# Optimization experiments

Hardware: AMD Instinct MI355X
Metric: run time of the kernel (lower is better)

## Reference

```python
import jax, jax.numpy as jnp
import numpy as np

HEADS = 16

def setup_inputs() -> dict:
    key = jax.random.key(0)
    ks = jax.random.split(key, 5)
    B, T, D = 2, 2048, 2048
    s = 0.02
    return {
        "x": jax.random.normal(ks[0], (B, T, D), dtype=jnp.float32),
        "Wq": jax.random.normal(ks[1], (D, D), dtype=jnp.float32) * s,
        "Wk": jax.random.normal(ks[2], (D, D), dtype=jnp.float32) * s,
        "Wv": jax.random.normal(ks[3], (D, D), dtype=jnp.float32) * s,
        "Wo": jax.random.normal(ks[4], (D, D), dtype=jnp.float32) * s,
    }

def reference(x, Wq, Wk, Wv, Wo):
    B, T, _ = x.shape
    H = HEADS
    Dh = Wq.shape[1] // H
    # projections: [B,T,H,Dh]
    q = (x @ Wq).reshape(B, T, H, Dh)
    k = (x @ Wk).reshape(B, T, H, Dh)
    v = (x @ Wv).reshape(B, T, H, Dh)
    # raw scores [B,H,T,T]
    scores = jnp.einsum("bthd,bshd->bhts", q, k)
    # NOTE (faithful to source): mask is multiplicative 0/1 tril (the
    # masked_fill(-inf) in the torch code is not in-place and has no effect),
    # and the scale is sqrt(token_len), not sqrt(head_dim).
    mask = jnp.tril(jnp.ones((T, T), dtype=scores.dtype))
    scores = scores * mask
    attn = jax.nn.softmax(scores / (T ** 0.5), axis=-1)
    out = jnp.einsum("bhts,bshd->bthd", attn, v).reshape(B, T, H * Dh)
    return out @ Wo
```

## Files before the change

### kernel.cpp

```cpp
#include <hip/hip_runtime.h>


typedef __attribute__((ext_vector_type(4))) float  f32x4;
typedef __attribute__((ext_vector_type(8))) short  bf16x8;
typedef __attribute__((ext_vector_type(4))) unsigned short u16x4;

#define AS1 __attribute__((address_space(1)))
#define AS3 __attribute__((address_space(3)))

__device__ __forceinline__ void llds16(const void* g, void* l) {
  __builtin_amdgcn_global_load_lds((const AS1 void*)g, (AS3 void*)l, 16, 0, 0);
}

__device__ __forceinline__ unsigned short f2bf(float f) {
  unsigned int u = __builtin_bit_cast(unsigned int, f);
  u += 0x7fffu + ((u >> 16) & 1u);
  return (unsigned short)(u >> 16);
}

__device__ __forceinline__ float bf2f(unsigned short u) {
  return __builtin_bit_cast(float, (unsigned int)u << 16);
}

__global__ __launch_bounds__(256) void cast_x_kernel(const float* __restrict__ in,
                                                     unsigned short* __restrict__ out) {
  int i = blockIdx.x * 256 + threadIdx.x;
  f32x4 v = ((const f32x4*)in)[i];
  u16x4 o;
  o[0] = f2bf(v[0]); o[1] = f2bf(v[1]); o[2] = f2bf(v[2]); o[3] = f2bf(v[3]);
  ((u16x4*)out)[i] = o;
}

__global__ __launch_bounds__(256) void transpose_w_kernel(const float* __restrict__ W,
                                                          unsigned short* __restrict__ Wt) {
  __shared__ float tile[32][33];
  const int bx = blockIdx.x << 5;
  const int by = blockIdx.y << 5;
  const int tx = threadIdx.x;
  const int ty = threadIdx.y;
#pragma unroll
  for (int r = ty; r < 32; r += 8)
    tile[r][tx] = W[(size_t)(bx + r) * 2048 + by + tx];
  __syncthreads();
#pragma unroll
  for (int r = ty; r < 32; r += 8)
    Wt[(size_t)(by + r) * 2048 + bx + tx] = f2bf(tile[tx][r]);
}

template <int OUT>
__global__ __launch_bounds__(512, 2) void gemm_bt(const unsigned short* __restrict__ A,
                                                  const unsigned short* __restrict__ Bt,
                                                  void* __restrict__ Cv) {
  __shared__ __align__(16) char smem[98304];
  const int tid  = threadIdx.x;
  const int lane = tid & 63;
  const int w    = tid >> 6;
  const int f    = blockIdx.x;
  const int xcd  = f & 7;
  const int g    = f >> 3;
  const int bm   = ((xcd >> 1) << 3) + (g & 7);
  const int bn   = ((xcd & 1) << 2) + (g >> 3);
  const int wr = w >> 2, wc = w & 3;
  const int q16 = lane >> 4;
  const int l15 = lane & 15;

  const int aIdx = (w << 6) + lane;
  const int aRow = aIdx >> 2, aCph = aIdx & 3;
  const unsigned short* aSrc = A + (size_t)((bm << 7) + aRow) * 2048
                                 + ((aCph ^ ((aRow >> 1) & 3)) << 3);
  const int bRow0 = aIdx >> 2, bCph0 = aIdx & 3;
  const int bIdx1 = 512 + aIdx;
  const int bRow1 = bIdx1 >> 2, bCph1 = bIdx1 & 3;
  const unsigned short* bSrc0 = Bt + (size_t)((bn << 8) + bRow0) * 2048
                                  + ((bCph0 ^ ((bRow0 >> 1) & 3)) << 3);
  const unsigned short* bSrc1 = Bt + (size_t)((bn << 8) + bRow1) * 2048
                                  + ((bCph1 ^ ((bRow1 >> 1) & 3)) << 3);

  const int swx = ((q16 ^ ((l15 >> 1) & 3)) << 4);
  const int aoff = ((wr << 6) + l15) * 64 + swx;
  const int boff = 8192 + ((wc << 6) + l15) * 64 + swx;

  f32x4 acc[4][4];
#pragma unroll
  for (int i = 0; i < 4; ++i)
#pragma unroll
    for (int j = 0; j < 4; ++j) acc[i][j] = (f32x4){0.f, 0.f, 0.f, 0.f};

  auto stageT = [&](int t, int slot) {
    char* sb = smem + slot * 24576 + (w << 10);
    const size_t ko = (size_t)t << 5;
    llds16(aSrc + ko, sb);
    llds16(bSrc0 + ko, sb + 8192);
    llds16(bSrc1 + ko, sb + 16384);
  };

  auto computeT = [&](int slot) {
    const char* base = smem + slot * 24576;
    bf16x8 af[4], bf[4];
#pragma unroll
    for (int mi = 0; mi < 4; ++mi) af[mi] = *(const bf16x8*)(base + aoff + (mi << 10));
#pragma unroll
    for (int ni = 0; ni < 4; ++ni) bf[ni] = *(const bf16x8*)(base + boff + (ni << 10));
    __builtin_amdgcn_s_setprio(1);
#pragma unroll
    for (int mi = 0; mi < 4; ++mi)
#pragma unroll
      for (int ni = 0; ni < 4; ++ni)
        acc[mi][ni] = __builtin_amdgcn_mfma_f32_16x16x32_bf16(af[mi], bf[ni], acc[mi][ni], 0, 0, 0);
    __builtin_amdgcn_s_setprio(0);
  };

  stageT(0, 0); stageT(1, 1); stageT(2, 2);

#pragma unroll 1
  for (int i = 0; i < 60; i += 4) {
#pragma unroll
    for (int u = 0; u < 4; ++u) {
      stageT(i + u + 3, (u + 3) & 3);
      asm volatile("s_waitcnt vmcnt(9)" ::: "memory");
      __builtin_amdgcn_s_barrier();
      computeT(u);
      __builtin_amdgcn_s_barrier();
    }
  }
  stageT(63, 3);
  asm volatile("s_waitcnt vmcnt(9)" ::: "memory");
  __builtin_amdgcn_s_barrier();
  computeT(0);
  __builtin_amdgcn_s_barrier();
  asm volatile("s_waitcnt vmcnt(6)" ::: "memory");
  __builtin_amdgcn_s_barrier();
  computeT(1);
  __builtin_amdgcn_s_barrier();
  asm volatile("s_waitcnt vmcnt(3)" ::: "memory");
  __builtin_amdgcn_s_barrier();
  computeT(2);
  __builtin_amdgcn_s_barrier();
  asm volatile("s_waitcnt vmcnt(0)" ::: "memory");
  __builtin_amdgcn_s_barrier();
  computeT(3);

  const int rb = q16 << 2;
#pragma unroll
  for (int mi = 0; mi < 4; ++mi) {
    int m0 = (bm << 7) + (wr << 6) + (mi << 4) + rb;
#pragma unroll
    for (int ni = 0; ni < 4; ++ni) {
      int n = (bn << 8) + (wc << 6) + (ni << 4) + l15;
      if constexpr (OUT == 0) {
        unsigned short* C = (unsigned short*)Cv;
#pragma unroll
        for (int j = 0; j < 4; ++j)
          C[(size_t)(m0 + j) * 2048 + n] = f2bf(acc[mi][ni][j]);
      } else if constexpr (OUT == 1) {
        u16x4 pk;
#pragma unroll
        for (int j = 0; j < 4; ++j) pk[j] = f2bf(acc[mi][ni][j]);
        int b = m0 >> 11, t = m0 & 2047;
        unsigned short* C = (unsigned short*)Cv;
        *(u16x4*)(C + ((size_t)((b << 4) + (n >> 7)) * 128 + (n & 127)) * 2048 + t) = pk;
      } else {
        float* C = (float*)Cv;
#pragma unroll
        for (int j = 0; j < 4; ++j)
          C[(size_t)(m0 + j) * 2048 + n] = acc[mi][ni][j];
      }
    }
  }
}

__global__ __launch_bounds__(256) void vsuf_kernel(const unsigned short* __restrict__ Vt,
                                                   float* __restrict__ Suf) {
  const int row  = blockIdx.x * 4 + (threadIdx.x >> 6);
  const int lane = threadIdx.x & 63;
  const unsigned short* vp = Vt + (size_t)row * 2048 + (lane << 5);
  float a = 0.f;
#pragma unroll
  for (int c = 0; c < 4; ++c) {
    bf16x8 v = *(const bf16x8*)(vp + (c << 3));
#pragma unroll
    for (int j = 0; j < 8; ++j) a += bf2f((unsigned short)v[j]);
  }
  float I = a;
#pragma unroll
  for (int off = 1; off < 64; off <<= 1) {
    float t = __shfl_down(I, off, 64);
    I += (lane + off < 64) ? t : 0.f;
  }
  Suf[(size_t)lane * 4096 + row] = I;
  if (lane == 0) Suf[(size_t)64 * 4096 + row] = 0.f;
}

__global__ __launch_bounds__(256) void attn_kernel(const unsigned short* __restrict__ Q,
                                                   const unsigned short* __restrict__ K,
                                                   const unsigned short* __restrict__ V,
                                                   const float* __restrict__ Suf,
                                                   unsigned short* __restrict__ O) {
  __shared__ __align__(16) char smem[36864];
  const int tid  = threadIdx.x;
  const int lane = tid & 63;
  const int w    = tid >> 6;
  const int q16  = lane >> 4;
  const int l15  = lane & 15;
  const int f    = blockIdx.x;
  const int bh    = ((f & 7) << 2) + ((f >> 3) & 3);
  const int strip = 31 - (f >> 5);
  const int b  = bh >> 4;
  const float scale = 0.02209708691207961f;
  const size_t qkbase = ((size_t)(b << 11)) * 2048 + ((size_t)(bh & 15) << 7);
  const size_t vbase  = (size_t)bh << 18;
  const int rb = q16 << 2;
  char* Psm = smem + 32768 + (w << 10);

  const int numIter = 2 * strip + 2;
  const int t0 = (strip << 6) + (w << 4);

  auto stage = [&](int s0, int kb, int vb) {
#pragma unroll
    for (int c = 0; c < 2; ++c) {
      int ch = (w << 1) + c;
      int rowK = (ch << 2) + q16;
      int colbK = (l15 << 4) ^ ((rowK & 7) << 4);
      llds16(K + qkbase + (size_t)(s0 + rowK) * 2048 + (colbK >> 1), smem + kb + (ch << 10));
      int rowV = (ch << 4) + (lane >> 2);
      int colbV = ((lane & 3) << 4) ^ (((rowV >> 2) & 3) << 4);
      llds16(V + vbase + (size_t)rowV * 2048 + s0 + (colbV >> 1), smem + vb + (ch << 10));
    }
  };

  bf16x8 qf[4];
  {
    const unsigned short* qp = Q + qkbase + (size_t)(t0 + l15) * 2048 + (q16 << 3);
#pragma unroll
    for (int kk = 0; kk < 4; ++kk) qf[kk] = *(const bf16x8*)(qp + (kk << 5));
  }

  f32x4 oacc[8];
#pragma unroll
  for (int i = 0; i < 8; ++i) oacc[i] = (f32x4){0.f, 0.f, 0.f, 0.f};
  float ell[4] = {0.f, 0.f, 0.f, 0.f};

  stage(0, 0, 16384);
  asm volatile("s_waitcnt vmcnt(0)" ::: "memory");
  __syncthreads();

  int cur = 0;
  for (int it = 0; it < numIter; ++it) {
    const int s0 = it << 5;
    if (it + 1 < numIter)
      stage(s0 + 32, (cur ^ 1) << 13, 16384 + ((cur ^ 1) << 13));

    if (s0 <= t0) {
      const int kb = cur << 13;
      const int vb = 16384 + (cur << 13);

      f32x4 sA = (f32x4){0.f, 0.f, 0.f, 0.f}, sB = (f32x4){0.f, 0.f, 0.f, 0.f};
#pragma unroll
      for (int kk = 0; kk < 4; ++kk) {
        int r0 = l15;
        bf16x8 k0f = *(const bf16x8*)(smem + kb + (r0 << 8) + (((kk << 6) + (q16 << 4)) ^ ((r0 & 7) << 4)));
        sA = __builtin_amdgcn_mfma_f32_16x16x32_bf16(qf[kk], k0f, sA, 0, 0, 0);
        int r1 = 16 + l15;
        bf16x8 k1f = *(const bf16x8*)(smem + kb + (r1 << 8) + (((kk << 6) + (q16 << 4)) ^ ((r1 & 7) << 4)));
        sB = __builtin_amdgcn_mfma_f32_16x16x32_bf16(qf[kk], k1f, sB, 0, 0, 0);
      }

      float pA[4], pB[4];
#pragma unroll
      for (int j = 0; j < 4; ++j) {
        int t  = t0 + rb + j;
        int sa = s0 + l15;
        float vA = (sa <= t)      ? sA[j] * scale : 0.f;
        float vB = (sa + 16 <= t) ? sB[j] * scale : 0.f;
        pA[j] = __expf(vA);
        pB[j] = __expf(vB);
        ell[j] += pA[j] + pB[j];
      }

#pragma unroll
      for (int j = 0; j < 4; ++j) {
        int r   = rb + j;
        int swz = ((r >> 1) & 3) << 4;
        *(unsigned short*)(Psm + (r << 6) + ((l15 << 1) ^ swz))        = f2bf(pA[j]);
        *(unsigned short*)(Psm + (r << 6) + ((32 + (l15 << 1)) ^ swz)) = f2bf(pB[j]);
      }
      asm volatile("s_waitcnt lgkmcnt(0)" ::: "memory");

      bf16x8 pa;
      {
        int r = l15;
        pa = *(const bf16x8*)(Psm + (r << 6) + ((q16 << 4) ^ (((r >> 1) & 3) << 4)));
      }
#pragma unroll
      for (int ni = 0; ni < 8; ++ni) {
        int dr = (ni << 4) + l15;
        bf16x8 vbf = *(const bf16x8*)(smem + vb + (dr << 6) + ((q16 << 4) ^ (((dr >> 2) & 3) << 4)));
        oacc[ni] = __builtin_amdgcn_mfma_f32_16x16x32_bf16(pa, vbf, oacc[ni], 0, 0, 0);
      }
    }

    asm volatile("s_waitcnt vmcnt(0)" ::: "memory");
    __syncthreads();
    cur ^= 1;
  }

  const int send = (t0 & ~31) + 32;
  const float* sp = Suf + (size_t)(send >> 5) * 4096 + ((size_t)bh << 7);
  const float extra = (float)(2048 - send);
#pragma unroll
  for (int ni = 0; ni < 8; ++ni) {
    float sv = sp[(ni << 4) + l15];
#pragma unroll
    for (int j = 0; j < 4; ++j) oacc[ni][j] += sv;
  }

#pragma unroll
  for (int j = 0; j < 4; ++j) {
    float r = ell[j];
    r += __shfl_xor(r, 1, 64);
    r += __shfl_xor(r, 2, 64);
    r += __shfl_xor(r, 4, 64);
    r += __shfl_xor(r, 8, 64);
    float inv = 1.0f / (r + extra);
    int t = t0 + rb + j;
    unsigned short* op = O + qkbase + (size_t)t * 2048;
#pragma unroll
    for (int ni = 0; ni < 8; ++ni)
      op[(ni << 4) + l15] = f2bf(oacc[ni][j] * inv);
  }
}

extern "C" void kernel_launch(void* const* d_in, const int* in_sizes, int n_in,
                              void* d_out, int out_size, void* d_ws, size_t ws_size,
                              hipStream_t stream) {
  (void)in_sizes; (void)n_in; (void)out_size; (void)ws_size;
  const float* x  = (const float*)d_in[0];
  const float* Wq = (const float*)d_in[1];
  const float* Wk = (const float*)d_in[2];
  const float* Wv = (const float*)d_in[3];
  const float* Wo = (const float*)d_in[4];
  float* out = (float*)d_out;

  char* ws = (char*)d_ws;
  unsigned short* Xb  = (unsigned short*)(ws);
  unsigned short* Wqt = (unsigned short*)(ws + 16777216);
  unsigned short* Wkt = (unsigned short*)(ws + 16777216 + 8388608);
  unsigned short* Wvt = (unsigned short*)(ws + 16777216 + 2 * 8388608);
  unsigned short* Wot = (unsigned short*)(ws + 16777216 + 3 * 8388608);
  unsigned short* Qb  = (unsigned short*)(ws + 50331648);
  unsigned short* Kb  = (unsigned short*)(ws + 67108864);
  unsigned short* Vt  = (unsigned short*)(ws + 83886080);
  unsigned short* Ob  = Xb;
  float*          Suf = (float*)Wqt;

  cast_x_kernel<<<8192, 256, 0, stream>>>(x, Xb);
  {
    dim3 tb(32, 8), tg(64, 64);
    transpose_w_kernel<<<tg, tb, 0, stream>>>(Wq, Wqt);
    transpose_w_kernel<<<tg, tb, 0, stream>>>(Wk, Wkt);
    transpose_w_kernel<<<tg, tb, 0, stream>>>(Wv, Wvt);
    transpose_w_kernel<<<tg, tb, 0, stream>>>(Wo, Wot);
  }
  gemm_bt<0><<<256, 512, 0, stream>>>(Xb, Wqt, (void*)Qb);
  gemm_bt<0><<<256, 512, 0, stream>>>(Xb, Wkt, (void*)Kb);
  gemm_bt<1><<<256, 512, 0, stream>>>(Xb, Wvt, (void*)Vt);

  vsuf_kernel<<<1024, 256, 0, stream>>>(Vt, Suf);

  attn_kernel<<<1024, 256, 0, stream>>>(Qb, Kb, Vt, Suf, Ob);

  gemm_bt<2><<<256, 512, 0, stream>>>(Ob, Wot, (void*)out);
}
```

Baseline: 273.4 us.

## Fuse QKV GEMMs and weight transposes, pipeline GEMM frags, fold scale into Q

Merges the three Q/K/V projection GEMMs into a single 768-block launch. This relies on Wqt/Wkt/Wvt being contiguous so they act as one 6144-row B matrix, with each block routing its epilogue to Q, K or V by region. The four weight transposes become one launch with a z dimension. The GEMM main loop is restructured to use one barrier per step and double-buffered register fragments, so the LDS reads for the next tile overlap the MFMAs of the current one. Attention takes the score scale from Q (pre-scaled in the GEMM epilogue), skips the causal mask on fully unmasked tiles, and uses a cheaper round-half-up bf16 conversion for P, which slightly changes rounding and adds Q quantization of the scaled values.

```diff
diff --git a/kernel.cpp b/kernel.cpp
--- a/kernel.cpp
+++ b/kernel.cpp
@@ -16,6 +16,10 @@
   unsigned int u = __builtin_bit_cast(unsigned int, f);
   u += 0x7fffu + ((u >> 16) & 1u);
   return (unsigned short)(u >> 16);
+}
+
+__device__ __forceinline__ unsigned short f2bfru(float f) {
+  return (unsigned short)((__builtin_bit_cast(unsigned int, f) + 0x8000u) >> 16);
 }
 
 __device__ __forceinline__ float bf2f(unsigned short u) {
@@ -31,9 +35,15 @@
   ((u16x4*)out)[i] = o;
 }
 
-__global__ __launch_bounds__(256) void transpose_w_kernel(const float* __restrict__ W,
-                                                          unsigned short* __restrict__ Wt) {
+__global__ __launch_bounds__(256) void transpose_w4_kernel(
+    const float* __restrict__ W0, const float* __restrict__ W1,
+    const float* __restrict__ W2, const float* __restrict__ W3,
+    unsigned short* __restrict__ T0, unsigned short* __restrict__ T1,
+    unsigned short* __restrict__ T2, unsigned short* __restrict__ T3) {
   __shared__ float tile[32][33];
+  const int z = blockIdx.z;
+  const float* W = (z == 0) ? W0 : (z == 1) ? W1 : (z == 2) ? W2 : W3;
+  unsigned short* Wt = (z == 0) ? T0 : (z == 1) ? T1 : (z == 2) ? T2 : T3;
   const int bx = blockIdx.x << 5;
   const int by = blockIdx.y << 5;
   const int tx = threadIdx.x;
@@ -47,10 +57,13 @@
     Wt[(size_t)(by + r) * 2048 + bx + tx] = f2bf(tile[tx][r]);
 }
 
-template <int OUT>
-__global__ __launch_bounds__(512, 2) void gemm_bt(const unsigned short* __restrict__ A,
-                                                  const unsigned short* __restrict__ Bt,
-                                                  void* __restrict__ Cv) {
+template <int EPI>
+__global__ __launch_bounds__(512, 2) void gemm_pipe(const unsigned short* __restrict__ A,
+                                                    const unsigned short* __restrict__ Bt,
+                                                    unsigned short* __restrict__ Qb,
+                                                    unsigned short* __restrict__ Kb,
+                                                    unsigned short* __restrict__ Vt,
+                                                    float* __restrict__ Co) {
   __shared__ __align__(16) char smem[98304];
   const int tid  = threadIdx.x;
   const int lane = tid & 63;
@@ -58,8 +71,9 @@
   const int f    = blockIdx.x;
   const int xcd  = f & 7;
   const int g    = f >> 3;
-  const int bm   = ((xcd >> 1) << 3) + (g & 7);
-  const int bn   = ((xcd & 1) << 2) + (g >> 3);
+  int bm, bn;
+  if constexpr (EPI == 0) { bn = xcd * 3 + (g % 3); bm = g / 3; }
+  else                    { bn = xcd;              bm = g;      }
   const int wr = w >> 2, wc = w & 3;
   const int q16 = lane >> 4;
   const int l15 = lane & 15;
@@ -68,15 +82,14 @@
   const int aRow = aIdx >> 2, aCph = aIdx & 3;
   const unsigned short* aSrc = A + (size_t)((bm << 7) + aRow) * 2048
                                  + ((aCph ^ ((aRow >> 1) & 3)) << 3);
-  const int bRow0 = aIdx >> 2, bCph0 = aIdx & 3;
+  const unsigned short* bSrc0 = Bt + (size_t)((bn << 8) + aRow) * 2048
+                                  + ((aCph ^ ((aRow >> 1) & 3)) << 3);
   const int bIdx1 = 512 + aIdx;
   const int bRow1 = bIdx1 >> 2, bCph1 = bIdx1 & 3;
-  const unsigned short* bSrc0 = Bt + (size_t)((bn << 8) + bRow0) * 2048
-                                  + ((bCph0 ^ ((bRow0 >> 1) & 3)) << 3);
   const unsigned short* bSrc1 = Bt + (size_t)((bn << 8) + bRow1) * 2048
                                   + ((bCph1 ^ ((bRow1 >> 1) & 3)) << 3);
 
-  const int swx = ((q16 ^ ((l15 >> 1) & 3)) << 4);
+  const int swx  = ((q16 ^ ((l15 >> 1) & 3)) << 4);
   const int aoff = ((wr << 6) + l15) * 64 + swx;
   const int boff = 8192 + ((wc << 6) + l15) * 64 + swx;
 
@@ -94,13 +107,15 @@
     llds16(bSrc1 + ko, sb + 16384);
   };
 
-  auto computeT = [&](int slot) {
+  bf16x8 fa0[4], fb0[4], fa1[4], fb1[4];
+  auto readFrags = [&](int slot, bf16x8* af, bf16x8* bf) {
     const char* base = smem + slot * 24576;
-    bf16x8 af[4], bf[4];
 #pragma unroll
     for (int mi = 0; mi < 4; ++mi) af[mi] = *(const bf16x8*)(base + aoff + (mi << 10));
 #pragma unroll
     for (int ni = 0; ni < 4; ++ni) bf[ni] = *(const bf16x8*)(base + boff + (ni << 10));
+  };
+  auto mfmaStep = [&](bf16x8* af, bf16x8* bf) {
     __builtin_amdgcn_s_setprio(1);
 #pragma unroll
     for (int mi = 0; mi < 4; ++mi)
@@ -109,61 +124,65 @@
         acc[mi][ni] = __builtin_amdgcn_mfma_f32_16x16x32_bf16(af[mi], bf[ni], acc[mi][ni], 0, 0, 0);
     __builtin_amdgcn_s_setprio(0);
   };
+  auto pipeStep = [&](int u, bf16x8* ca, bf16x8* cb, bf16x8* na, bf16x8* nb) {
+    asm volatile("s_waitcnt vmcnt(3)" ::: "memory");
+    asm volatile("s_barrier" ::: "memory");
+    stageT(u + 3, (u + 3) & 3);
+    readFrags((u + 1) & 3, na, nb);
+    mfmaStep(ca, cb);
+  };
 
   stageT(0, 0); stageT(1, 1); stageT(2, 2);
-
+  asm volatile("s_waitcnt vmcnt(6)" ::: "memory");
+  asm volatile("s_barrier" ::: "memory");
+  readFrags(0, fa0, fb0);
+
+  pipeStep(0, fa0, fb0, fa1, fb1);
 #pragma unroll 1
-  for (int i = 0; i < 60; i += 4) {
-#pragma unroll
-    for (int u = 0; u < 4; ++u) {
-      stageT(i + u + 3, (u + 3) & 3);
-      asm volatile("s_waitcnt vmcnt(9)" ::: "memory");
-      __builtin_amdgcn_s_barrier();
-      computeT(u);
-      __builtin_amdgcn_s_barrier();
-    }
-  }
-  stageT(63, 3);
-  asm volatile("s_waitcnt vmcnt(9)" ::: "memory");
-  __builtin_amdgcn_s_barrier();
-  computeT(0);
-  __builtin_amdgcn_s_barrier();
-  asm volatile("s_waitcnt vmcnt(6)" ::: "memory");
-  __builtin_amdgcn_s_barrier();
-  computeT(1);
-  __builtin_amdgcn_s_barrier();
+  for (int u = 1; u < 61; u += 2) {
+    pipeStep(u,     fa1, fb1, fa0, fb0);
+    pipeStep(u + 1, fa0, fb0, fa1, fb1);
+  }
   asm volatile("s_waitcnt vmcnt(3)" ::: "memory");
-  __builtin_amdgcn_s_barrier();
-  computeT(2);
-  __builtin_amdgcn_s_barrier();
+  asm volatile("s_barrier" ::: "memory");
+  readFrags(2, fa0, fb0);
+  mfmaStep(fa1, fb1);
   asm volatile("s_waitcnt vmcnt(0)" ::: "memory");
-  __builtin_amdgcn_s_barrier();
-  computeT(3);
-
+  asm volatile("s_barrier" ::: "memory");
+  readFrags(3, fa1, fb1);
+  mfmaStep(fa0, fb0);
+  mfmaStep(fa1, fb1);
+
+  const float qscale = 0.02209708691207961f;
   const int rb = q16 << 2;
 #pragma unroll
   for (int mi = 0; mi < 4; ++mi) {
     int m0 = (bm << 7) + (wr << 6) + (mi << 4) + rb;
 #pragma unroll
     for (int ni = 0; ni < 4; ++ni) {
-      int n = (bn << 8) + (wc << 6) + (ni << 4) + l15;
-      if constexpr (OUT == 0) {
-        unsigned short* C = (unsigned short*)Cv;
+      if constexpr (EPI == 0) {
+        int region = bn >> 3;
+        int nloc = ((bn & 7) << 8) + (wc << 6) + (ni << 4) + l15;
+        if (region == 0) {
+#pragma unroll
+          for (int j = 0; j < 4; ++j)
+            Qb[(size_t)(m0 + j) * 2048 + nloc] = f2bf(acc[mi][ni][j] * qscale);
+        } else if (region == 1) {
+#pragma unroll
+          for (int j = 0; j < 4; ++j)
+            Kb[(size_t)(m0 + j) * 2048 + nloc] = f2bf(acc[mi][ni][j]);
+        } else {
+          u16x4 pk;
+#pragma unroll
+          for (int j = 0; j < 4; ++j) pk[j] = f2bf(acc[mi][ni][j]);
+          int b = m0 >> 11, t = m0 & 2047;
+          *(u16x4*)(Vt + ((size_t)((b << 4) + (nloc >> 7)) * 128 + (nloc & 127)) * 2048 + t) = pk;
+        }
+      } else {
+        int n = (bn << 8) + (wc << 6) + (ni << 4) + l15;
 #pragma unroll
         for (int j = 0; j < 4; ++j)
-          C[(size_t)(m0 + j) * 2048 + n] = f2bf(acc[mi][ni][j]);
-      } else if constexpr (OUT == 1) {
-        u16x4 pk;
-#pragma unroll
-        for (int j = 0; j < 4; ++j) pk[j] = f2bf(acc[mi][ni][j]);
-        int b = m0 >> 11, t = m0 & 2047;
-        unsigned short* C = (unsigned short*)Cv;
-        *(u16x4*)(C + ((size_t)((b << 4) + (n >> 7)) * 128 + (n & 127)) * 2048 + t) = pk;
-      } else {
-        float* C = (float*)Cv;
-#pragma unroll
-        for (int j = 0; j < 4; ++j)
-          C[(size_t)(m0 + j) * 2048 + n] = acc[mi][ni][j];
+          Co[(size_t)(m0 + j) * 2048 + n] = acc[mi][ni][j];
       }
     }
   }
@@ -206,7 +225,6 @@
   const int bh    = ((f & 7) << 2) + ((f >> 3) & 3);
   const int strip = 31 - (f >> 5);
   const int b  = bh >> 4;
-  const float scale = 0.02209708691207961f;
   const size_t qkbase = ((size_t)(b << 11)) * 2048 + ((size_t)(bh & 15) << 7);
   const size_t vbase  = (size_t)bh << 18;
   const int rb = q16 << 2;
@@ -266,23 +284,32 @@
       }
 
       float pA[4], pB[4];
-#pragma unroll
-      for (int j = 0; j < 4; ++j) {
-        int t  = t0 + rb + j;
-        int sa = s0 + l15;
-        float vA = (sa <= t)      ? sA[j] * scale : 0.f;
-        float vB = (sa + 16 <= t) ? sB[j] * scale : 0.f;
-        pA[j] = __expf(vA);
-        pB[j] = __expf(vB);
-        ell[j] += pA[j] + pB[j];
+      if (s0 + 31 <= t0) {
+#pragma unroll
+        for (int j = 0; j < 4; ++j) {
+          pA[j] = __expf(sA[j]);
+          pB[j] = __expf(sB[j]);
+          ell[j] += pA[j] + pB[j];
+        }
+      } else {
+#pragma unroll
+        for (int j = 0; j < 4; ++j) {
+          int t  = t0 + rb + j;
+          int sa = s0 + l15;
+          float vA = (sa <= t)      ? sA[j] : 0.f;
+          float vB = (sa + 16 <= t) ? sB[j] : 0.f;
+          pA[j] = __expf(vA);
+          pB[j] = __expf(vB);
+          ell[j] += pA[j] + pB[j];
+        }
       }
 
 #pragma unroll
       for (int j = 0; j < 4; ++j) {
         int r   = rb + j;
         int swz = ((r >> 1) & 3) << 4;
-        *(unsigned short*)(Psm + (r << 6) + ((l15 << 1) ^ swz))        = f2bf(pA[j]);
-        *(unsigned short*)(Psm + (r << 6) + ((32 + (l15 << 1)) ^ swz)) = f2bf(pB[j]);
+        *(unsigned short*)(Psm + (r << 6) + ((l15 << 1) ^ swz))        = f2bfru(pA[j]);
+        *(unsigned short*)(Psm + (r << 6) + ((32 + (l15 << 1)) ^ swz)) = f2bfru(pB[j]);
       }
       asm volatile("s_waitcnt lgkmcnt(0)" ::: "memory");
 
@@ -355,19 +382,14 @@
 
   cast_x_kernel<<<8192, 256, 0, stream>>>(x, Xb);
   {
-    dim3 tb(32, 8), tg(64, 64);
-    transpose_w_kernel<<<tg, tb, 0, stream>>>(Wq, Wqt);
-    transpose_w_kernel<<<tg, tb, 0, stream>>>(Wk, Wkt);
-    transpose_w_kernel<<<tg, tb, 0, stream>>>(Wv, Wvt);
-    transpose_w_kernel<<<tg, tb, 0, stream>>>(Wo, Wot);
-  }
-  gemm_bt<0><<<256, 512, 0, stream>>>(Xb, Wqt, (void*)Qb);
-  gemm_bt<0><<<256, 512, 0, stream>>>(Xb, Wkt, (void*)Kb);
-  gemm_bt<1><<<256, 512, 0, stream>>>(Xb, Wvt, (void*)Vt);
+    dim3 tb(32, 8), tg(64, 64, 4);
+    transpose_w4_kernel<<<tg, tb, 0, stream>>>(Wq, Wk, Wv, Wo, Wqt, Wkt, Wvt, Wot);
+  }
+  gemm_pipe<0><<<768, 512, 0, stream>>>(Xb, Wqt, Qb, Kb, Vt, nullptr);
 
   vsuf_kernel<<<1024, 256, 0, stream>>>(Vt, Suf);
 
   attn_kernel<<<1024, 256, 0, stream>>>(Qb, Kb, Vt, Suf, Ob);
 
-  gemm_bt<2><<<256, 512, 0, stream>>>(Ob, Wot, (void*)out);
-}
+  gemm_pipe<1><<<256, 512, 0, stream>>>(Ob, Wot, nullptr, nullptr, nullptr, out);
+}
```

Measured after the change: 265.6 us. -2.8%, faster.
